# Performance work log

Hardware: AMD Instinct MI355X
Metric: run time of the kernel (lower is better)

Reference implementation:

```python
import jax, jax.numpy as jnp
import numpy as np

N = 50_000      # node_num
E = 1_600_000   # n_edges (avg degree 32)
D = 256         # input feature dim
H = 128         # GCN / hidden units
FC = 1024       # fc0 units
C = 16          # num_classes


def _tn(key, shape, std=0.1):
    # truncated normal in [-2, 2] std, matching tf.random.truncated_normal(stddev=0.1)
    return jax.random.truncated_normal(key, -2.0, 2.0, shape, jnp.float32) * std


def setup_inputs() -> dict:
    key = jax.random.key(0)
    ks = jax.random.split(key, 16)
    return {
        "x": jax.random.normal(ks[0], (N, D), jnp.float32),
        "edge_index": jax.random.randint(ks[1], (2, E), 0, N, jnp.int32),
        # GCN layer params (tfg GCN: kernel + bias)
        "gcn0_W": _tn(ks[2], (D, H)), "gcn0_b": jnp.zeros((H,), jnp.float32),
        "gcn1_W": _tn(ks[3], (H, H)), "gcn1_b": jnp.zeros((H,), jnp.float32),
        "gcn2_W": _tn(ks[4], (H, H)), "gcn2_b": jnp.zeros((H,), jnp.float32),
        # extra dense block between gcn10 and gcn11
        "w1": _tn(ks[5], (H, H)), "b1": _tn(ks[6], (N, H)),
        # fc head
        "fc0_W": _tn(ks[7], (H, FC)), "fc0_b": jnp.zeros((FC,), jnp.float32),
        "fc1_W": _tn(ks[8], (FC, C)), "fc1_b": jnp.zeros((C,), jnp.float32),
    }


def reference(x, edge_index, gcn0_W, gcn0_b, gcn1_W, gcn1_b, gcn2_W, gcn2_b,
              w1, b1, fc0_W, fc0_b, fc1_W, fc1_b):
    n = x.shape[0]
    src, dst = edge_index[0], edge_index[1]
    loops = jnp.arange(n, dtype=src.dtype)
    # GCN renormalization trick: A_hat = A + I, w_ij = deg_i^-1/2 * deg_j^-1/2
    src_f = jnp.concatenate([src, loops])   # [E+N]
    dst_f = jnp.concatenate([dst, loops])
    deg = jax.ops.segment_sum(jnp.ones(src_f.shape[0], jnp.float32), src_f, num_segments=n)
    norm = jnp.where(deg > 0, deg, 1.0) ** -0.5
    ew = norm[src_f] * norm[dst_f]          # [E+N]

    def gcn(h, W, b):
        h = h @ W                                                      # [N,H]
        agg = jax.ops.segment_sum(h[src_f] * ew[:, None], dst_f, num_segments=n)
        return agg + b

    h1 = jax.nn.relu(gcn(x, gcn0_W, gcn0_b))       # gcn10, relu
    h11 = jax.nn.relu(h1 @ w1 + b1)                # dense with per-node bias
    h2 = gcn(h11, gcn1_W, gcn1_b)                  # gcn11, no activation
    h2 = jax.nn.relu(gcn(h2, gcn2_W, gcn2_b))      # gcn12, relu
    h = h1 + h2
    h = jax.nn.relu(h @ fc0_W + fc0_b)             # fc0
    return h @ fc1_W + fc1_b                       # fc1 logits [N,C]
```

## Files before the change

kernel.cpp:

```cpp
#include <hip/hip_runtime.h>
#include <hip/hip_bf16.h>
#include <hip/hip_fp16.h>
#include <cstddef>
#include <cstdint>

#define NNODES 50000
#define NEDGES 1600000
#define DIM 256
#define HID 128
#define FCU 1024
#define NCLS 16

#define NBKT 256
#define BW 196
#define NBLK_A 64
#define EPB (NEDGES / NBLK_A)
#define CAPB 8192

#define DCHUNK 12800
#define DSLICE 64
#define DEPB (NEDGES / DSLICE)

typedef short s16x8 __attribute__((ext_vector_type(8)));
typedef _Float16 f16x8 __attribute__((ext_vector_type(8)));
typedef float f32x4 __attribute__((ext_vector_type(4)));
#define MFMA16 __builtin_amdgcn_mfma_f32_16x16x32_bf16
#define MFMAH  __builtin_amdgcn_mfma_f32_16x16x32_f16

typedef unsigned short u16;
typedef unsigned int u32;

__device__ inline u16 f2bf(float f) {
    u32 u = __float_as_uint(f);
    return (u16)((u + 0x7FFF + ((u >> 16) & 1)) >> 16);
}
__device__ inline float bf2f(u16 h) { return __uint_as_float(((u32)h) << 16); }
__device__ inline void split2(float v, u16& h, u16& l) {
    h = f2bf(v);
    l = f2bf(v - bf2f(h));
}


__global__ __launch_bounds__(256) void histDeg(const int* __restrict__ ei, int* __restrict__ degS) {
    __shared__ int h[DCHUNK];
    int chunk = blockIdx.x >> 6;
    int slice = blockIdx.x & (DSLICE - 1);
    int t = threadIdx.x;
    int base0 = chunk * DCHUNK;
    for (int i = t; i < DCHUNK; i += 256) h[i] = 0;
    __syncthreads();
    int base = slice * DEPB;
    for (int e = base + t; e < base + DEPB; e += 256) {
        int s = ei[e] - base0;
        if ((unsigned)s < (unsigned)DCHUNK) atomicAdd(&h[s], 1);
    }
    __syncthreads();
    int lim = NNODES - base0; if (lim > DCHUNK) lim = DCHUNK;
    for (int i = t; i < lim; i += 256) {
        int v = h[i];
        if (v) atomicAdd(&degS[base0 + i], v);
    }
}

__global__ void norm_kernel(const int* __restrict__ degS, float* __restrict__ nrm) {
    int i = blockIdx.x * blockDim.x + threadIdx.x;
    if (i < NNODES) nrm[i] = rsqrtf((float)(degS[i] + 1));
}

__global__ __launch_bounds__(1024) void histA(const int* __restrict__ ei, int* __restrict__ hist) {
    __shared__ int h[NBKT];
    int blk = blockIdx.x, t = threadIdx.x;
    if (t < NBKT) h[t] = 0;
    __syncthreads();
    int base = blk * EPB;
    for (int e = base + t; e < base + EPB; e += 1024) {
        int dst = ei[NEDGES + e];
        atomicAdd(&h[dst / BW], 1);
    }
    __syncthreads();
    if (t < NBKT) hist[t * NBLK_A + blk] = h[t];
}

__global__ __launch_bounds__(1024) void scanh_a(int* __restrict__ hist, int* __restrict__ bsum) {
    __shared__ int s[1024];
    int b = blockIdx.x, t = threadIdx.x, i = b * 1024 + t;
    int v = hist[i];
    s[t] = v;
    __syncthreads();
    for (int off = 1; off < 1024; off <<= 1) {
        int x = (t >= off) ? s[t - off] : 0;
        __syncthreads();
        s[t] += x;
        __syncthreads();
    }
    hist[i] = s[t] - v;
    if (t == 1023) bsum[b] = s[1023];
}
__global__ void scanh_b(int* __restrict__ bsum) {
    if (threadIdx.x == 0 && blockIdx.x == 0) {
        int a = 0;
        for (int j = 0; j < 16; ++j) { int t = bsum[j]; bsum[j] = a; a += t; }
    }
}
__global__ __launch_bounds__(1024) void scanh_c(int* __restrict__ hist, const int* __restrict__ bsum) {
    int i = blockIdx.x * 1024 + threadIdx.x;
    hist[i] += bsum[blockIdx.x];
}

__global__ __launch_bounds__(1024) void bucket_fill(const int* __restrict__ ei,
                                                    const int* __restrict__ hist,
                                                    u32* __restrict__ packed) {
    __shared__ int cur[NBKT];
    int blk = blockIdx.x, t = threadIdx.x;
    if (t < NBKT) cur[t] = hist[t * NBLK_A + blk];
    __syncthreads();
    int base = blk * EPB;
    for (int e = base + t; e < base + EPB; e += 1024) {
        int src = ei[e], dst = ei[NEDGES + e];
        int p = atomicAdd(&cur[dst / BW], 1);
        packed[p] = ((u32)dst << 16) | (u32)src;
    }
}

__global__ __launch_bounds__(256) void bucket_csr(const u32* __restrict__ packed,
                                                  const int* __restrict__ hist,
                                                  int* __restrict__ rowptr, u16* __restrict__ csr) {
    __shared__ u32 st[CAPB];
    __shared__ u16 so[CAPB];
    __shared__ int cnt[256], excl[256];
    int b = blockIdx.x, t = threadIdx.x;
    int ebase = hist[b * NBLK_A];
    int eend  = (b < NBKT - 1) ? hist[(b + 1) * NBLK_A] : NEDGES;
    int nE = eend - ebase;
    if (nE > CAPB) nE = CAPB;
    cnt[t] = 0;
    __syncthreads();
    for (int i = t; i < nE; i += 256) {
        u32 p = packed[ebase + i];
        st[i] = p;
        atomicAdd(&cnt[(int)(p >> 16) - b * BW], 1);
    }
    __syncthreads();
    int v = cnt[t];
    excl[t] = v;
    __syncthreads();
    for (int off = 1; off < 256; off <<= 1) {
        int x = (t >= off) ? excl[t - off] : 0;
        __syncthreads();
        excl[t] += x;
        __syncthreads();
    }
    int ex = excl[t] - v;
    int node = b * BW + t;
    if (t < BW && node < NNODES) rowptr[node] = ebase + ex;
    if (b == NBKT - 1 && t == 0) rowptr[NNODES] = NEDGES;
    cnt[t] = ex;
    __syncthreads();
    for (int i = t; i < nE; i += 256) {
        u32 p = st[i];
        int pos = atomicAdd(&cnt[(int)(p >> 16) - b * BW], 1);
        so[pos] = (u16)(p & 0xFFFF);
    }
    __syncthreads();
    for (int i = t; i < nE; i += 256) csr[ebase + i] = so[i];
}


__global__ __launch_bounds__(256) void conv_x(const float* __restrict__ x,
                                              u16* __restrict__ xh, u16* __restrict__ xl) {
    int i = blockIdx.x * blockDim.x + threadIdx.x;
    const float4 v = *reinterpret_cast<const float4*>(x + (size_t)i * 4);
    u16 h0, l0, h1, l1, h2, l2, h3, l3;
    split2(v.x, h0, l0); split2(v.y, h1, l1); split2(v.z, h2, l2); split2(v.w, h3, l3);
    ushort4 hv = make_ushort4(h0, h1, h2, h3), lv = make_ushort4(l0, l1, l2, l3);
    *reinterpret_cast<ushort4*>(xh + (size_t)i * 4) = hv;
    *reinterpret_cast<ushort4*>(xl + (size_t)i * 4) = lv;
}

__global__ __launch_bounds__(256) void conv_wT(const float* __restrict__ W, int K, int N,
                                               u16* __restrict__ outH, u16* __restrict__ outL) {
    int o = blockIdx.x * blockDim.x + threadIdx.x;
    if (o < K * N) {
        int n = o / K, k = o - n * K;
        u16 h, l;
        split2(W[(size_t)k * N + n], h, l);
        outH[o] = h; outL[o] = l;
    }
}

__global__ __launch_bounds__(256) void conv_w1h(const float* __restrict__ W, __half* __restrict__ outT) {
    int o = blockIdx.x * blockDim.x + threadIdx.x;
    if (o < FCU * NCLS) {
        int n = o / FCU, k = o - n * FCU;
        outT[o] = __float2half(W[(size_t)k * NCLS + n]);
    }
}


template<int VAR, int WLO>
__global__ __launch_bounds__(256) void agg_fast(
    const __half* __restrict__ g, const float* __restrict__ nrm,
    const int* __restrict__ rowptr, const u16* __restrict__ csr,
    const float* __restrict__ bias,
    const u16* __restrict__ h1H, const u16* __restrict__ h1L,
    u16* __restrict__ outH, u16* __restrict__ outL)
{
    int w = threadIdx.x >> 6, lane = threadIdx.x & 63;
    int i = blockIdx.x * 4 + w;
    if (i >= NNODES) return;
    const __half2* gp = reinterpret_cast<const __half2*>(g);
    size_t lrow = (size_t)i * 64 + lane;
    float2 acc = __half22float2(gp[lrow]);
    int e0 = rowptr[i], e1 = rowptr[i + 1];
    int e = e0;
    for (; e + 8 <= e1; e += 8) {
        int s[8];
#pragma unroll
        for (int q = 0; q < 8; ++q) s[q] = csr[e + q];
        __half2 v[8];
#pragma unroll
        for (int q = 0; q < 8; ++q) v[q] = gp[(size_t)s[q] * 64 + lane];
#pragma unroll
        for (int q = 0; q < 8; ++q) {
            float2 f = __half22float2(v[q]);
            acc.x += f.x; acc.y += f.y;
        }
    }
    for (; e < e1; ++e) {
        int s = csr[e];
        float2 f = __half22float2(gp[(size_t)s * 64 + lane]);
        acc.x += f.x; acc.y += f.y;
    }
    float ni = nrm[i];
    const float2 b = *reinterpret_cast<const float2*>(bias + lane * 2);
    float v0 = fmaf(ni, acc.x, b.x);
    float v1 = fmaf(ni, acc.y, b.y);
    if (VAR != 1) { v0 = fmaxf(v0, 0.f); v1 = fmaxf(v1, 0.f); }
    if (VAR == 2) {
        ushort2 rh = *reinterpret_cast<const ushort2*>(h1H + (size_t)i * HID + lane * 2);
        ushort2 rl = *reinterpret_cast<const ushort2*>(h1L + (size_t)i * HID + lane * 2);
        v0 += bf2f(rh.x) + bf2f(rl.x);
        v1 += bf2f(rh.y) + bf2f(rl.y);
    }
    if (WLO) {
        u16 h0, l0, h1v, l1v;
        split2(v0, h0, l0);
        split2(v1, h1v, l1v);
        *reinterpret_cast<ushort2*>(outH + (size_t)i * HID + lane * 2) = make_ushort2(h0, h1v);
        *reinterpret_cast<ushort2*>(outL + (size_t)i * HID + lane * 2) = make_ushort2(l0, l1v);
    } else {
        *reinterpret_cast<ushort2*>(outH + (size_t)i * HID + lane * 2) = make_ushort2(f2bf(v0), f2bf(v1));
    }
}


template<int K, int MODE, int PL>
__global__ __launch_bounds__(256) void gemm_split(
    const u16* __restrict__ Ah, const u16* __restrict__ Al,
    const u16* __restrict__ BTh, const u16* __restrict__ BTl,
    const float* __restrict__ pnb, const float* __restrict__ nrmv,
    __half* __restrict__ outG, u16* __restrict__ outH, u16* __restrict__ outL, int M)
{
    const int PK = 40;
    __shared__ __align__(16) u16 AsH[64 * PK];
    __shared__ __align__(16) u16 BsH[128 * PK];
    __shared__ __align__(16) u16 AsL[PL == 3 ? 64 * PK : 1];
    __shared__ __align__(16) u16 BsL[PL == 3 ? 128 * PK : 1];
    int tid = threadIdx.x, lane = tid & 63, w = tid >> 6;
    int wr = w >> 1, wc = w & 1;
    int l15 = lane & 15, l4 = lane >> 4;
    int blockRow = blockIdx.x * 64;
    f32x4 acc[2][4] = {};

    for (int kk = 0; kk < K; kk += 32) {
        {
            int row = tid >> 2, kc = (tid & 3) * 8;
            int gr = blockRow + row; if (gr >= M) gr = M - 1;
            *(s16x8*)&AsH[row * PK + kc] = *(const s16x8*)&Ah[(size_t)gr * K + kk + kc];
            if (PL == 3)
                *(s16x8*)&AsL[row * PK + kc] = *(const s16x8*)&Al[(size_t)gr * K + kk + kc];
        }
#pragma unroll
        for (int i2 = 0; i2 < 2; ++i2) {
            int idx = tid + i2 * 256;
            int n = idx >> 2, kc = (idx & 3) * 8;
            *(s16x8*)&BsH[n * PK + kc] = *(const s16x8*)&BTh[(size_t)n * K + kk + kc];
            if (PL == 3)
                *(s16x8*)&BsL[n * PK + kc] = *(const s16x8*)&BTl[(size_t)n * K + kk + kc];
        }
        __syncthreads();
        s16x8 ah[2], al[2], bh[4], bl[4];
#pragma unroll
        for (int mi = 0; mi < 2; ++mi) {
            ah[mi] = *(const s16x8*)&AsH[(wr * 32 + mi * 16 + l15) * PK + 8 * l4];
            if (PL == 3) al[mi] = *(const s16x8*)&AsL[(wr * 32 + mi * 16 + l15) * PK + 8 * l4];
        }
#pragma unroll
        for (int ni = 0; ni < 4; ++ni) {
            bh[ni] = *(const s16x8*)&BsH[(wc * 64 + ni * 16 + l15) * PK + 8 * l4];
            if (PL == 3) bl[ni] = *(const s16x8*)&BsL[(wc * 64 + ni * 16 + l15) * PK + 8 * l4];
        }
#pragma unroll
        for (int mi = 0; mi < 2; ++mi)
#pragma unroll
            for (int ni = 0; ni < 4; ++ni) {
                acc[mi][ni] = MFMA16(ah[mi], bh[ni], acc[mi][ni], 0, 0, 0);
                if (PL == 3) {
                    acc[mi][ni] = MFMA16(ah[mi], bl[ni], acc[mi][ni], 0, 0, 0);
                    acc[mi][ni] = MFMA16(al[mi], bh[ni], acc[mi][ni], 0, 0, 0);
                }
            }
        __syncthreads();
    }
#pragma unroll
    for (int mi = 0; mi < 2; ++mi)
#pragma unroll
        for (int ni = 0; ni < 4; ++ni) {
            int c = wc * 64 + ni * 16 + l15;
#pragma unroll
            for (int j = 0; j < 4; ++j) {
                int r = blockRow + wr * 32 + mi * 16 + l4 * 4 + j;
                if (r < M) {
                    if (MODE == 0) {
                        outG[(size_t)r * 128 + c] = __float2half(nrmv[r] * acc[mi][ni][j]);
                    } else {
                        float v = fmaxf(acc[mi][ni][j] + pnb[(size_t)r * 128 + c], 0.f);
                        if (MODE == 1) {
                            u16 h, l;
                            split2(v, h, l);
                            outH[(size_t)r * 128 + c] = h;
                            outL[(size_t)r * 128 + c] = l;
                        } else {
                            outH[(size_t)r * 128 + c] = f2bf(v);
                        }
                    }
                }
            }
        }
}


__global__ __launch_bounds__(256) void fc_kernel(
    const u16* __restrict__ Ahi,
    const u16* __restrict__ BTh,
    const float* __restrict__ fc0b,
    const __half* __restrict__ W1f,
    const float* __restrict__ fc1b,
    float* __restrict__ out, int M)
{
    __shared__ __align__(16) u16 vs[32 * 128];
    __shared__ __align__(16) u16 W1s[16 * 128];
    int tid = threadIdx.x, lane = tid & 63, w = tid >> 6;
    int l15 = lane & 15, l4 = lane >> 4;
    int blockRow = blockIdx.x * 32;

    s16x8 ahr[2][4];
#pragma unroll
    for (int mi = 0; mi < 2; ++mi) {
        int r = blockRow + mi * 16 + l15; if (r >= M) r = M - 1;
#pragma unroll
        for (int ks = 0; ks < 4; ++ks)
            ahr[mi][ks] = *(const s16x8*)&Ahi[(size_t)r * HID + ks * 32 + 8 * l4];
    }

    f32x4 acc2 = {0.f, 0.f, 0.f, 0.f};
    s16x8 bcur[2][4];
#pragma unroll
    for (int ni = 0; ni < 2; ++ni)
#pragma unroll
        for (int ks = 0; ks < 4; ++ks)
            bcur[ni][ks] = *(const s16x8*)&BTh[(size_t)(w * 32 + ni * 16 + l15) * HID + ks * 32 + 8 * l4];

#pragma unroll
    for (int cc = 0; cc < FCU / 128; ++cc) {
        int co = cc * 128;
        s16x8 bnxt[2][4];
        if (cc + 1 < FCU / 128) {
#pragma unroll
            for (int ni = 0; ni < 2; ++ni)
#pragma unroll
                for (int ks = 0; ks < 4; ++ks)
                    bnxt[ni][ks] = *(const s16x8*)&BTh[(size_t)(co + 128 + w * 32 + ni * 16 + l15) * HID + ks * 32 + 8 * l4];
        }

        f32x4 acc[2][2] = {};
#pragma unroll
        for (int ks = 0; ks < 4; ++ks)
#pragma unroll
            for (int mi = 0; mi < 2; ++mi)
#pragma unroll
                for (int ni = 0; ni < 2; ++ni)
                    acc[mi][ni] = MFMA16(ahr[mi][ks], bcur[ni][ks], acc[mi][ni], 0, 0, 0);

        {
            int cls = tid >> 4, kc = (tid & 15) * 8;
            s16x8 t = *(const s16x8*)&W1f[(size_t)cls * FCU + co + kc];
            *(s16x8*)&W1s[cls * 128 + (kc ^ ((cls & 7) << 3))] = t;
        }
#pragma unroll
        for (int mi = 0; mi < 2; ++mi)
#pragma unroll
            for (int ni = 0; ni < 2; ++ni) {
                int unit = w * 32 + ni * 16 + l15;
                float b0v = fc0b[co + unit];
#pragma unroll
                for (int j = 0; j < 4; ++j) {
                    int rl = mi * 16 + l4 * 4 + j;
                    float v = fmaxf(acc[mi][ni][j] + b0v, 0.f);
                    vs[rl * 128 + (unit ^ ((rl & 7) << 3))] = __half_as_ushort(__float2half(v));
                }
            }
        __syncthreads();

        if (w < 2) {
#pragma unroll
            for (int ks = 0; ks < 4; ++ks) {
                int row = w * 16 + l15;
                int colk = ks * 32 + 8 * l4;
                f16x8 a2 = *(const f16x8*)&vs[row * 128 + (colk ^ ((row & 7) << 3))];
                f16x8 b2 = *(const f16x8*)&W1s[l15 * 128 + (colk ^ ((l15 & 7) << 3))];
                acc2 = MFMAH(a2, b2, acc2, 0, 0, 0);
            }
        }
        __syncthreads();

        if (cc + 1 < FCU / 128) {
#pragma unroll
            for (int ni = 0; ni < 2; ++ni)
#pragma unroll
                for (int ks = 0; ks < 4; ++ks)
                    bcur[ni][ks] = bnxt[ni][ks];
        }
    }

    if (w < 2) {
#pragma unroll
        for (int j = 0; j < 4; ++j) {
            int gr = blockRow + w * 16 + l4 * 4 + j;
            if (gr < M) out[(size_t)gr * NCLS + l15] = acc2[j] + fc1b[l15];
        }
    }
}


extern "C" void kernel_launch(void* const* d_in, const int* in_sizes, int n_in,
                              void* d_out, int out_size, void* d_ws, size_t ws_size,
                              hipStream_t stream)
{
    const float* x     = (const float*)d_in[0];
    const int*   ei    = (const int*)d_in[1];
    const float* gcn0W = (const float*)d_in[2];
    const float* gcn0b = (const float*)d_in[3];
    const float* gcn1W = (const float*)d_in[4];
    const float* gcn1b = (const float*)d_in[5];
    const float* gcn2W = (const float*)d_in[6];
    const float* gcn2b = (const float*)d_in[7];
    const float* w1    = (const float*)d_in[8];
    const float* b1    = (const float*)d_in[9];
    const float* fc0W  = (const float*)d_in[10];
    const float* fc0b  = (const float*)d_in[11];
    const float* fc1W  = (const float*)d_in[12];
    const float* fc1b  = (const float*)d_in[13];
    float* out = (float*)d_out;

    char* ws = (char*)d_ws;
    size_t off = 0;
    auto alloc = [&](size_t bytes) -> void* {
        void* p = ws + off;
        off = (off + bytes + 255) & ~(size_t)255;
        return p;
    };
    int* degS   = (int*)alloc((size_t)NNODES * 4);
    int* rowptr = (int*)alloc((size_t)(NNODES + 1) * 4);
    int* hist   = (int*)alloc((size_t)NBKT * NBLK_A * 4);
    int* bsum   = (int*)alloc(64 * 4);
    u32* packed = (u32*)alloc((size_t)NEDGES * 4);
    u16* csr    = (u16*)alloc((size_t)NEDGES * 2);
    float* nrm  = (float*)alloc((size_t)NNODES * 4);
    u16* W0Th = (u16*)alloc((size_t)DIM * HID * 2);  u16* W0Tl = (u16*)alloc((size_t)DIM * HID * 2);
    u16* w1Th = (u16*)alloc((size_t)HID * HID * 2);  u16* w1Tl = (u16*)alloc((size_t)HID * HID * 2);
    u16* W1Th = (u16*)alloc((size_t)HID * HID * 2);  u16* W1Tl = (u16*)alloc((size_t)HID * HID * 2);
    u16* W2Th = (u16*)alloc((size_t)HID * HID * 2);  u16* W2Tl = (u16*)alloc((size_t)HID * HID * 2);
    u16* F0Th = (u16*)alloc((size_t)HID * FCU * 2);  u16* F0Tl = (u16*)alloc((size_t)HID * FCU * 2);
    __half* W1f = (__half*)alloc((size_t)FCU * NCLS * 2);
    __half* bufG = (__half*)alloc((size_t)NNODES * HID * 2);
    u16* R1 = (u16*)alloc((size_t)2 * NNODES * DIM * 2);
    u16* xh = R1, *xl = R1 + (size_t)NNODES * DIM;
    u16* h1H = R1,                            *h1L = R1 + (size_t)NNODES * HID;
    u16* B3H = R1 + (size_t)2 * NNODES * HID, *B3L = R1 + (size_t)3 * NNODES * HID;
    (void)B3L;

    const int M = NNODES;
    hipMemsetAsync(degS, 0, (size_t)NNODES * 4, stream);

    histDeg<<<4 * DSLICE, 256, 0, stream>>>(ei, degS);
    norm_kernel<<<(NNODES + 255) / 256, 256, 0, stream>>>(degS, nrm);
    histA<<<NBLK_A, 1024, 0, stream>>>(ei, hist);
    scanh_a<<<16, 1024, 0, stream>>>(hist, bsum);
    scanh_b<<<1, 64, 0, stream>>>(bsum);
    scanh_c<<<16, 1024, 0, stream>>>(hist, bsum);
    bucket_fill<<<NBLK_A, 1024, 0, stream>>>(ei, hist, packed);
    bucket_csr<<<NBKT, 256, 0, stream>>>(packed, hist, rowptr, csr);

    conv_x<<<(NNODES * DIM / 4 + 255) / 256, 256, 0, stream>>>(x, xh, xl);
    conv_wT<<<(DIM * HID + 255) / 256, 256, 0, stream>>>(gcn0W, DIM, HID, W0Th, W0Tl);
    conv_wT<<<(HID * HID + 255) / 256, 256, 0, stream>>>(w1,    HID, HID, w1Th, w1Tl);
    conv_wT<<<(HID * HID + 255) / 256, 256, 0, stream>>>(gcn1W, HID, HID, W1Th, W1Tl);
    conv_wT<<<(HID * HID + 255) / 256, 256, 0, stream>>>(gcn2W, HID, HID, W2Th, W2Tl);
    conv_wT<<<(HID * FCU + 255) / 256, 256, 0, stream>>>(fc0W,  HID, FCU, F0Th, F0Tl);
    conv_w1h<<<(FCU * NCLS + 255) / 256, 256, 0, stream>>>(fc1W, W1f);

    const int GB = (M + 63) / 64;
    const int GB32 = (M + 31) / 32;
    const int AB = (NNODES + 3) / 4;
    gemm_split<DIM, 0, 3><<<GB, 256, 0, stream>>>(xh, xl, W0Th, W0Tl, nullptr, nrm, bufG, nullptr, nullptr, M);
    agg_fast<0, 1><<<AB, 256, 0, stream>>>(bufG, nrm, rowptr, csr, gcn0b, nullptr, nullptr, h1H, h1L);
    gemm_split<HID, 2, 1><<<GB, 256, 0, stream>>>(h1H, nullptr, w1Th, nullptr, b1, nullptr, nullptr, B3H, nullptr, M);
    gemm_split<HID, 0, 1><<<GB, 256, 0, stream>>>(B3H, nullptr, W1Th, nullptr, nullptr, nrm, bufG, nullptr, nullptr, M);
    agg_fast<1, 0><<<AB, 256, 0, stream>>>(bufG, nrm, rowptr, csr, gcn1b, nullptr, nullptr, B3H, nullptr);
    gemm_split<HID, 0, 1><<<GB, 256, 0, stream>>>(B3H, nullptr, W2Th, nullptr, nullptr, nrm, bufG, nullptr, nullptr, M);
    agg_fast<2, 0><<<AB, 256, 0, stream>>>(bufG, nrm, rowptr, csr, gcn2b, h1H, h1L, B3H, nullptr);
    fc_kernel<<<GB32, 256, 0, stream>>>(B3H, F0Th, fc0b, W1f, fc1b, out, M);
}
```

Before: 419.2 us.

## Split fc1 reduction across waves to remove per-chunk block barriers

Each wave now computes the fc1 partial product over its own 32 fc0 units per chunk, using a private LDS slice and reading W1 directly from global memory. This removes the two __syncthreads per chunk and the shared W1 staging, and avoids having only two of four waves do the second matmul. A single cross-wave reduction through LDS at the end sums the four partials. It also drops the register double-buffering of the B fragments in favour of per-k-step loads, which may expose more global load latency.

```diff
diff --git a/kernel.cpp b/kernel.cpp
--- a/kernel.cpp
+++ b/kernel.cpp
@@ -348,11 +348,12 @@
     const float* __restrict__ fc1b,
     float* __restrict__ out, int M)
 {
-    __shared__ __align__(16) u16 vs[32 * 128];
-    __shared__ __align__(16) u16 W1s[16 * 128];
+    __shared__ __align__(16) u16 vs[4 * 32 * 32];
+    __shared__ __align__(16) float redS[4 * 32 * 16];
     int tid = threadIdx.x, lane = tid & 63, w = tid >> 6;
     int l15 = lane & 15, l4 = lane >> 4;
     int blockRow = blockIdx.x * 32;
+    u16* vsw = vs + w * (32 * 32);
 
     s16x8 ahr[2][4];
 #pragma unroll
@@ -363,82 +364,59 @@
             ahr[mi][ks] = *(const s16x8*)&Ahi[(size_t)r * HID + ks * 32 + 8 * l4];
     }
 
-    f32x4 acc2 = {0.f, 0.f, 0.f, 0.f};
-    s16x8 bcur[2][4];
-#pragma unroll
-    for (int ni = 0; ni < 2; ++ni)
-#pragma unroll
-        for (int ks = 0; ks < 4; ++ks)
-            bcur[ni][ks] = *(const s16x8*)&BTh[(size_t)(w * 32 + ni * 16 + l15) * HID + ks * 32 + 8 * l4];
-
+    f32x4 acc2[2] = {};
 #pragma unroll
     for (int cc = 0; cc < FCU / 128; ++cc) {
-        int co = cc * 128;
-        s16x8 bnxt[2][4];
-        if (cc + 1 < FCU / 128) {
+        int ub = cc * 128 + w * 32;
+        f32x4 acc[2][2] = {};
+#pragma unroll
+        for (int ks = 0; ks < 4; ++ks) {
+            s16x8 bh[2];
 #pragma unroll
             for (int ni = 0; ni < 2; ++ni)
-#pragma unroll
-                for (int ks = 0; ks < 4; ++ks)
-                    bnxt[ni][ks] = *(const s16x8*)&BTh[(size_t)(co + 128 + w * 32 + ni * 16 + l15) * HID + ks * 32 + 8 * l4];
-        }
-
-        f32x4 acc[2][2] = {};
-#pragma unroll
-        for (int ks = 0; ks < 4; ++ks)
+                bh[ni] = *(const s16x8*)&BTh[(size_t)(ub + ni * 16 + l15) * HID + ks * 32 + 8 * l4];
 #pragma unroll
             for (int mi = 0; mi < 2; ++mi)
 #pragma unroll
                 for (int ni = 0; ni < 2; ++ni)
-                    acc[mi][ni] = MFMA16(ahr[mi][ks], bcur[ni][ks], acc[mi][ni], 0, 0, 0);
-
-        {
-            int cls = tid >> 4, kc = (tid & 15) * 8;
-            s16x8 t = *(const s16x8*)&W1f[(size_t)cls * FCU + co + kc];
-            *(s16x8*)&W1s[cls * 128 + (kc ^ ((cls & 7) << 3))] = t;
+                    acc[mi][ni] = MFMA16(ahr[mi][ks], bh[ni], acc[mi][ni], 0, 0, 0);
         }
 #pragma unroll
         for (int mi = 0; mi < 2; ++mi)
 #pragma unroll
             for (int ni = 0; ni < 2; ++ni) {
-                int unit = w * 32 + ni * 16 + l15;
-                float b0v = fc0b[co + unit];
+                int lc = ni * 16 + l15;
+                float b0v = fc0b[ub + lc];
 #pragma unroll
                 for (int j = 0; j < 4; ++j) {
                     int rl = mi * 16 + l4 * 4 + j;
                     float v = fmaxf(acc[mi][ni][j] + b0v, 0.f);
-                    vs[rl * 128 + (unit ^ ((rl & 7) << 3))] = __half_as_ushort(__float2half(v));
+                    int c = lc >> 3;
+                    vsw[rl * 32 + ((c ^ (rl & 3)) << 3) + (lc & 7)] =
+                        __half_as_ushort(__float2half(v));
                 }
             }
-        __syncthreads();
-
-        if (w < 2) {
-#pragma unroll
-            for (int ks = 0; ks < 4; ++ks) {
-                int row = w * 16 + l15;
-                int colk = ks * 32 + 8 * l4;
-                f16x8 a2 = *(const f16x8*)&vs[row * 128 + (colk ^ ((row & 7) << 3))];
-                f16x8 b2 = *(const f16x8*)&W1s[l15 * 128 + (colk ^ ((l15 & 7) << 3))];
-                acc2 = MFMAH(a2, b2, acc2, 0, 0, 0);
-            }
-        }
-        __syncthreads();
-
-        if (cc + 1 < FCU / 128) {
-#pragma unroll
-            for (int ni = 0; ni < 2; ++ni)
-#pragma unroll
-                for (int ks = 0; ks < 4; ++ks)
-                    bcur[ni][ks] = bnxt[ni][ks];
-        }
-    }
-
-    if (w < 2) {
-#pragma unroll
-        for (int j = 0; j < 4; ++j) {
-            int gr = blockRow + w * 16 + l4 * 4 + j;
-            if (gr < M) out[(size_t)gr * NCLS + l15] = acc2[j] + fc1b[l15];
-        }
+#pragma unroll
+        for (int mi = 0; mi < 2; ++mi) {
+            int row = mi * 16 + l15;
+            f16x8 a2 = *(const f16x8*)&vsw[row * 32 + ((l4 ^ (row & 3)) << 3)];
+            f16x8 b2 = *(const f16x8*)&W1f[(size_t)l15 * FCU + ub + 8 * l4];
+            acc2[mi] = MFMAH(a2, b2, acc2[mi], 0, 0, 0);
+        }
+    }
+
+#pragma unroll
+    for (int mi = 0; mi < 2; ++mi)
+#pragma unroll
+        for (int j = 0; j < 4; ++j)
+            redS[(w * 32 + mi * 16 + l4 * 4 + j) * 16 + l15] = acc2[mi][j];
+    __syncthreads();
+    for (int idx = tid; idx < 32 * 16; idx += 256) {
+        int r = idx >> 4, cls = idx & 15;
+        float s = redS[r * 16 + cls] + redS[(32 + r) * 16 + cls]
+                + redS[(64 + r) * 16 + cls] + redS[(96 + r) * 16 + cls];
+        int gr = blockRow + r;
+        if (gr < M) out[(size_t)gr * NCLS + cls] = s + fc1b[cls];
     }
 }
 
```

After: 425.4 us. About the same (+1.5%).
